# Performance work log

Hardware: AMD Instinct MI355X
Metric: run time of the kernel (lower is better)

## Reference

```python
import jax, jax.numpy as jnp
import numpy as np

GAMMA = 1.5
BN_EPS = 1e-5


def sparsemax(z):
    """Sparsemax along last axis (Martins & Astudillo, 2016)."""
    z = z - jnp.max(z, axis=-1, keepdims=True)
    z_sorted = -jnp.sort(-z, axis=-1)                      # descending sort
    z_cumsum = jnp.cumsum(z_sorted, axis=-1)
    k = jnp.arange(1, z.shape[-1] + 1, dtype=z.dtype)
    support = (z_sorted - (z_cumsum - 1.0) / k) > 0
    k_z = jnp.clip(jnp.sum(support, axis=-1, keepdims=True), 1, None).astype(z.dtype)
    idx = (k_z - 1.0).astype(jnp.int32)
    tau = (jnp.take_along_axis(z_cumsum, idx, axis=-1) - 1.0) / k_z
    return jnp.clip(z - tau, 0.0, None)


def setup_inputs() -> dict:
    key = jax.random.key(0)
    k1, k2 = jax.random.split(key)
    B, T, E, H = 32, 512, 512, 8
    x = jax.random.normal(k1, (B, T, E), dtype=jnp.float32)
    # torch Linear weight (out, in), kaiming-ish scale
    W = jax.random.normal(k2, (H, E, E), dtype=jnp.float32) / np.float32(np.sqrt(E))
    bn_weight = jnp.ones((H, E), dtype=jnp.float32)
    bn_bias = jnp.zeros((H, E), dtype=jnp.float32)
    return {"x": x, "W": W, "bn_weight": bn_weight, "bn_bias": bn_bias}


def reference(x, W, bn_weight, bn_bias):
    B, T, E = x.shape
    H = W.shape[0]
    gi = x.reshape(B * T, E)
    # all-head linear: y[n,o] = sum_i gi[n,i] * W[h,o,i]
    logits = jnp.einsum('ni,hoi->hno', gi, W)              # (H, B*T, E)
    # BatchNorm1d in training mode: batch stats over the B*T axis, biased var
    mean = jnp.mean(logits, axis=1, keepdims=True)
    var = jnp.var(logits, axis=1, keepdims=True)
    logits = (logits - mean) / jnp.sqrt(var + BN_EPS)
    logits = logits * bn_weight[:, None, :] + bn_bias[:, None, :]
    logits = logits.reshape(H, B, T, E)

    prior0 = jnp.ones((B, T, E), dtype=x.dtype)

    def step(prior, logits_h):
        mask_h = sparsemax(logits_h * prior)
        prior = prior * jnp.clip(GAMMA - mask_h, 0.0, None)
        return prior, mask_h

    _, masks = jax.lax.scan(step, prior0, logits)          # masks: (H, B, T, E)
    masked_xs = x[None, :, :, :] * masks                   # (H, B, T, E)
    return masked_xs, jnp.transpose(masks, (1, 0, 2, 3))   # (B, H, T, E)
```

## Files before the change

kernel.cpp:

```cpp
#include <hip/hip_runtime.h>
#include <stdint.h>

#define Hh 8
#define Bb 32
#define Tt 512
#define Ee 512
#define Nn 16384
#define GAMMA_ 1.5f
#define BN_EPS_ 1e-5f

typedef _Float16 f16x4 __attribute__((ext_vector_type(4)));
typedef _Float16 f16x8 __attribute__((ext_vector_type(8)));
typedef float    f32x4 __attribute__((ext_vector_type(4)));

__device__ __forceinline__ void async_ld16(void* lds, const void* g) {
    __builtin_amdgcn_global_load_lds(
        (const __attribute__((address_space(1))) void*)g,
        (__attribute__((address_space(3))) void*)lds, 16, 0, 0);
}

__device__ __forceinline__ float dpp_sum64(float v) {
    int t;
    t = __builtin_amdgcn_update_dpp(0, __float_as_int(v), 0x111, 0xf, 0xf, true);
    v += __int_as_float(t);
    t = __builtin_amdgcn_update_dpp(0, __float_as_int(v), 0x112, 0xf, 0xf, true);
    v += __int_as_float(t);
    t = __builtin_amdgcn_update_dpp(0, __float_as_int(v), 0x114, 0xf, 0xf, true);
    v += __int_as_float(t);
    t = __builtin_amdgcn_update_dpp(0, __float_as_int(v), 0x118, 0xf, 0xf, true);
    v += __int_as_float(t);
    t = __builtin_amdgcn_update_dpp(0, __float_as_int(v), 0x142, 0xf, 0xf, true);
    v += __int_as_float(t);
    t = __builtin_amdgcn_update_dpp(0, __float_as_int(v), 0x143, 0xf, 0xf, true);
    v += __int_as_float(t);
    return __int_as_float(__builtin_amdgcn_readlane(__float_as_int(v), 63));
}

__global__ __launch_bounds__(256) void cvt_kernel(const float* __restrict__ x,
                                                  const float* __restrict__ W,
                                                  _Float16* __restrict__ xh,
                                                  _Float16* __restrict__ wh) {
    const int NX = Bb * Tt * Ee;
    int i = (blockIdx.x * 256 + threadIdx.x) * 4;
    if (i < NX) {
        float4 v = *(const float4*)(x + i);
        f16x4 o = {(_Float16)v.x, (_Float16)v.y, (_Float16)v.z, (_Float16)v.w};
        *(f16x4*)(xh + i) = o;
    } else {
        int j = i - NX;
        float4 v = *(const float4*)(W + j);
        f16x4 o = {(_Float16)v.x, (_Float16)v.y, (_Float16)v.z, (_Float16)v.w};
        *(f16x4*)(wh + j) = o;
    }
}

__global__ __launch_bounds__(256) void gemm_kernel(const _Float16* __restrict__ A,
                                                   const _Float16* __restrict__ Bm,
                                                   _Float16* __restrict__ C,
                                                   float* __restrict__ sums,
                                                   float* __restrict__ sumsq) {
    __shared__ alignas(16) _Float16 As[2][128 * 32];
    __shared__ alignas(16) _Float16 Bs[2][128 * 32];
    const int id = blockIdx.x;
    const int g  = id >> 5;
    const int r  = id & 31;
    const int h  = g >> 4;
    const int q  = r & 7;
    const int s  = r >> 3;
    const int mb = ((g & 15) * 8 + (q & 3) * 2 + (s & 1)) * 128;
    const int nb = ((q >> 2) * 2 + (s >> 1)) * 128;

    const int t    = threadIdx.x;
    const int lane = t & 63;
    const int w    = t >> 6;
    const int wm   = (w >> 1) * 64;
    const int wn   = (w & 1) * 64;
    const int quad = lane >> 4;
    const int l16  = lane & 15;

    const int kc = ((t & 3) - ((t >> 3) & 3)) & 3;
    const _Float16* Ap = A + (size_t)(mb + (t >> 2)) * Ee + kc * 8;
    const _Float16* Bp = Bm + (size_t)h * Ee * Ee + (size_t)(nb + (t >> 2)) * Ee + kc * 8;

    f32x4 acc[4][4] = {};

    async_ld16(&As[0][t * 8],        Ap);
    async_ld16(&As[0][2048 + t * 8], Ap + 64 * Ee);
    async_ld16(&Bs[0][t * 8],        Bp);
    async_ld16(&Bs[0][2048 + t * 8], Bp + 64 * Ee);

    const int so = ((quad + (l16 >> 1)) & 3) * 8;

    int buf = 0;
    for (int k0 = 0; k0 < Ee; k0 += 32) {
        __syncthreads();
        if (k0 + 32 < Ee) {
            int nb2 = buf ^ 1;
            async_ld16(&As[nb2][t * 8],        Ap + k0 + 32);
            async_ld16(&As[nb2][2048 + t * 8], Ap + 64 * Ee + k0 + 32);
            async_ld16(&Bs[nb2][t * 8],        Bp + k0 + 32);
            async_ld16(&Bs[nb2][2048 + t * 8], Bp + 64 * Ee + k0 + 32);
        }
        f16x8 a8[4], b8[4];
#pragma unroll
        for (int mt = 0; mt < 4; ++mt)
            a8[mt] = *(const f16x8*)(&As[buf][(wm + mt * 16 + l16) * 32 + so]);
#pragma unroll
        for (int nt = 0; nt < 4; ++nt)
            b8[nt] = *(const f16x8*)(&Bs[buf][(wn + nt * 16 + l16) * 32 + so]);
#pragma unroll
        for (int mt = 0; mt < 4; ++mt)
#pragma unroll
            for (int nt = 0; nt < 4; ++nt)
                acc[mt][nt] = __builtin_amdgcn_mfma_f32_16x16x32_f16(a8[mt], b8[nt], acc[mt][nt], 0, 0, 0);
        buf ^= 1;
    }

#pragma unroll
    for (int nt = 0; nt < 4; ++nt) {
        float sv = 0.f, ss = 0.f;
#pragma unroll
        for (int mt = 0; mt < 4; ++mt)
#pragma unroll
            for (int rr = 0; rr < 4; ++rr) { float v = acc[mt][nt][rr]; sv += v; ss += v * v; }
        sv += __shfl_xor(sv, 16, 64); sv += __shfl_xor(sv, 32, 64);
        ss += __shfl_xor(ss, 16, 64); ss += __shfl_xor(ss, 32, 64);
        if (quad == 0) {
            int col = nb + wn + nt * 16 + l16;
            atomicAdd(&sums[h * Ee + col], sv);
            atomicAdd(&sumsq[h * Ee + col], ss);
        }
    }

    _Float16* Cp = C + (size_t)h * Nn * Ee;
#pragma unroll
    for (int mt = 0; mt < 4; ++mt)
#pragma unroll
        for (int rr = 0; rr < 4; ++rr) {
            int row = mb + wm + mt * 16 + quad * 4 + rr;
            size_t off = (size_t)row * Ee + nb + wn + l16;
#pragma unroll
            for (int nt = 0; nt < 4; ++nt)
                Cp[off + nt * 16] = (_Float16)acc[mt][nt][rr];
        }
}

__global__ __launch_bounds__(256) void stats_kernel(const float* __restrict__ sums,
                                                    const float* __restrict__ sumsq,
                                                    const float* __restrict__ bnw,
                                                    const float* __restrict__ bnb,
                                                    float* __restrict__ cA,
                                                    float* __restrict__ cB) {
    int i = blockIdx.x * 256 + threadIdx.x;
    float mean = sums[i] * (1.0f / Nn);
    float var  = sumsq[i] * (1.0f / Nn) - mean * mean;
    float inv  = rsqrtf(var + BN_EPS_);
    float a    = bnw[i] * inv;
    cA[i] = a;
    cB[i] = bnb[i] - mean * a;
}

__global__ __launch_bounds__(256) void rows_kernel(const float* __restrict__ x,
                                                   const _Float16* __restrict__ lg,
                                                   const float* __restrict__ cA,
                                                   const float* __restrict__ cB,
                                                   float* __restrict__ out) {
    const int n    = blockIdx.x * 4 + (threadIdx.x >> 6);
    const int lane = threadIdx.x & 63;
    const int e0   = lane * 4;
    const int bb   = n >> 9;
    const int tt   = n & 511;

    float xr[8], prior[8];
    {
        const float* xp = x + (size_t)n * Ee;
        float4 x0 = *(const float4*)(xp + e0);
        float4 x1 = *(const float4*)(xp + 256 + e0);
        xr[0]=x0.x; xr[1]=x0.y; xr[2]=x0.z; xr[3]=x0.w;
        xr[4]=x1.x; xr[5]=x1.y; xr[6]=x1.z; xr[7]=x1.w;
    }
#pragma unroll
    for (int j = 0; j < 8; ++j) prior[j] = 1.0f;

    float* omx = out;
    float* omk = out + (size_t)Hh * Nn * Ee;

    const _Float16* lrow = lg + (size_t)n * Ee;
    f16x4 l0 = *(const f16x4*)(lrow + e0);
    f16x4 l1 = *(const f16x4*)(lrow + 256 + e0);

#pragma unroll 1
    for (int h = 0; h < Hh; ++h) {
        f16x4 p0 = l0, p1 = l1;
        if (h + 1 < Hh) {
            const _Float16* lnx = lrow + (size_t)(h + 1) * Nn * Ee;
            p0 = *(const f16x4*)(lnx + e0);
            p1 = *(const f16x4*)(lnx + 256 + e0);
        }
        float z[8];
        {
            const float* ap = cA + h * Ee + e0;
            const float* bp = cB + h * Ee + e0;
            float4 a0 = *(const float4*)(ap);
            float4 b0 = *(const float4*)(bp);
            float4 a1 = *(const float4*)(ap + 256);
            float4 b1 = *(const float4*)(bp + 256);
            z[0] = ((float)l0[0] * a0.x + b0.x) * prior[0];
            z[1] = ((float)l0[1] * a0.y + b0.y) * prior[1];
            z[2] = ((float)l0[2] * a0.z + b0.z) * prior[2];
            z[3] = ((float)l0[3] * a0.w + b0.w) * prior[3];
            z[4] = ((float)l1[0] * a1.x + b1.x) * prior[4];
            z[5] = ((float)l1[1] * a1.y + b1.y) * prior[5];
            z[6] = ((float)l1[2] * a1.z + b1.z) * prior[6];
            z[7] = ((float)l1[3] * a1.w + b1.w) * prior[7];
        }

        float sl = 0.f;
#pragma unroll
        for (int j = 0; j < 8; ++j) sl += z[j];
        float tau = (dpp_sum64(sl) - 1.0f) * (1.0f / 512.0f);
        int cprev = 512;
#pragma unroll 1
        for (int it = 0; it < 64; ++it) {
            float s2 = 0.f;
            int cnt = 0;
#pragma unroll
            for (int j = 0; j < 8; ++j) {
                bool p = z[j] > tau;
                s2 += p ? z[j] : 0.0f;
                cnt += (int)__popcll(__ballot(p));
            }
            float S = dpp_sum64(s2);
            if (cnt == cprev) break;
            cprev = cnt;
            tau = (S - 1.0f) / (float)cnt;
        }

        size_t oxoff = ((size_t)h * Nn + n) * Ee + e0;
        size_t okoff = (((size_t)bb * Hh + h) * Tt + tt) * Ee + e0;
        f32x4 vx, vm;
#pragma unroll
        for (int j = 0; j < 4; ++j) {
            float m = fmaxf(z[j] - tau, 0.0f);
            prior[j] *= fmaxf(GAMMA_ - m, 0.0f);
            vm[j] = m; vx[j] = xr[j] * m;
        }
        __builtin_nontemporal_store(vx, (f32x4*)(omx + oxoff));
        __builtin_nontemporal_store(vm, (f32x4*)(omk + okoff));
#pragma unroll
        for (int j = 0; j < 4; ++j) {
            float m = fmaxf(z[4 + j] - tau, 0.0f);
            prior[4 + j] *= fmaxf(GAMMA_ - m, 0.0f);
            vm[j] = m; vx[j] = xr[4 + j] * m;
        }
        __builtin_nontemporal_store(vx, (f32x4*)(omx + oxoff + 256));
        __builtin_nontemporal_store(vm, (f32x4*)(omk + okoff + 256));
        l0 = p0; l1 = p1;
    }
}

extern "C" void kernel_launch(void* const* d_in, const int* in_sizes, int n_in,
                              void* d_out, int out_size, void* d_ws, size_t ws_size,
                              hipStream_t stream) {
    const float* x   = (const float*)d_in[0];
    const float* W   = (const float*)d_in[1];
    const float* bnw = (const float*)d_in[2];
    const float* bnb = (const float*)d_in[3];
    float* out = (float*)d_out;

    uint8_t* ws = (uint8_t*)d_ws;
    _Float16* xh = (_Float16*)(ws);
    _Float16* wh = (_Float16*)(ws + 16777216);
    _Float16* lg = (_Float16*)(ws + 20971520);
    float* sums  = (float*)(ws + 155189248);
    float* sumsq = (float*)(ws + 155205632);
    float* cA    = (float*)(ws + 155222016);
    float* cB    = (float*)(ws + 155238400);

    hipMemsetAsync(sums, 0, 2 * 4096 * sizeof(float), stream);

    cvt_kernel<<<10240, 256, 0, stream>>>(x, W, xh, wh);
    gemm_kernel<<<4096, 256, 0, stream>>>(xh, wh, lg, sums, sumsq);
    stats_kernel<<<16, 256, 0, stream>>>(sums, sumsq, bnw, bnb, cA, cB);
    rows_kernel<<<4096, 256, 0, stream>>>(x, lg, cA, cB, out);
}
```

Before: 671.8 us.

## Enlarge GEMM block tile to 256x256 with 512 threads and 128x64 warp tiles

The GEMM moves from a 128x128 block tile with 256 threads to a 256x256 block tile with 512 threads. Each wave now computes a 128x64 sub-tile with 8x4 MFMA accumulators, which raises reuse of each LDS load and cuts global/L2 traffic per FLOP. The cost is more accumulator registers (launch_bounds 512,2), more LDS per block, and fewer blocks (1024), which may lower occupancy. The L2-friendly block swizzle is also replaced with a simple linear mapping.

```diff
diff --git a/kernel.cpp b/kernel.cpp
--- a/kernel.cpp
+++ b/kernel.cpp
@@ -54,27 +54,24 @@
     }
 }
 
-__global__ __launch_bounds__(256) void gemm_kernel(const _Float16* __restrict__ A,
-                                                   const _Float16* __restrict__ Bm,
-                                                   _Float16* __restrict__ C,
-                                                   float* __restrict__ sums,
-                                                   float* __restrict__ sumsq) {
-    __shared__ alignas(16) _Float16 As[2][128 * 32];
-    __shared__ alignas(16) _Float16 Bs[2][128 * 32];
-    const int id = blockIdx.x;
-    const int g  = id >> 5;
-    const int r  = id & 31;
-    const int h  = g >> 4;
-    const int q  = r & 7;
-    const int s  = r >> 3;
-    const int mb = ((g & 15) * 8 + (q & 3) * 2 + (s & 1)) * 128;
-    const int nb = ((q >> 2) * 2 + (s >> 1)) * 128;
+__global__ __launch_bounds__(512, 2) void gemm_kernel(const _Float16* __restrict__ A,
+                                                      const _Float16* __restrict__ Bm,
+                                                      _Float16* __restrict__ C,
+                                                      float* __restrict__ sums,
+                                                      float* __restrict__ sumsq) {
+    __shared__ alignas(16) _Float16 As[2][256 * 32];
+    __shared__ alignas(16) _Float16 Bs[2][256 * 32];
+    const int id  = blockIdx.x;
+    const int h   = id >> 7;
+    const int rem = id & 127;
+    const int mb  = (rem >> 1) * 256;
+    const int nb  = (rem & 1) * 256;
 
     const int t    = threadIdx.x;
     const int lane = t & 63;
     const int w    = t >> 6;
-    const int wm   = (w >> 1) * 64;
-    const int wn   = (w & 1) * 64;
+    const int wrow = (w >> 2) * 128;
+    const int wcol = (w & 3) * 64;
     const int quad = lane >> 4;
     const int l16  = lane & 15;
 
@@ -82,12 +79,12 @@
     const _Float16* Ap = A + (size_t)(mb + (t >> 2)) * Ee + kc * 8;
     const _Float16* Bp = Bm + (size_t)h * Ee * Ee + (size_t)(nb + (t >> 2)) * Ee + kc * 8;
 
-    f32x4 acc[4][4] = {};
+    f32x4 acc[8][4] = {};
 
     async_ld16(&As[0][t * 8],        Ap);
-    async_ld16(&As[0][2048 + t * 8], Ap + 64 * Ee);
+    async_ld16(&As[0][4096 + t * 8], Ap + 128 * Ee);
     async_ld16(&Bs[0][t * 8],        Bp);
-    async_ld16(&Bs[0][2048 + t * 8], Bp + 64 * Ee);
+    async_ld16(&Bs[0][4096 + t * 8], Bp + 128 * Ee);
 
     const int so = ((quad + (l16 >> 1)) & 3) * 8;
 
@@ -95,24 +92,23 @@
     for (int k0 = 0; k0 < Ee; k0 += 32) {
         __syncthreads();
         if (k0 + 32 < Ee) {
-            int nb2 = buf ^ 1;
-            async_ld16(&As[nb2][t * 8],        Ap + k0 + 32);
-            async_ld16(&As[nb2][2048 + t * 8], Ap + 64 * Ee + k0 + 32);
-            async_ld16(&Bs[nb2][t * 8],        Bp + k0 + 32);
-            async_ld16(&Bs[nb2][2048 + t * 8], Bp + 64 * Ee + k0 + 32);
-        }
-        f16x8 a8[4], b8[4];
-#pragma unroll
-        for (int mt = 0; mt < 4; ++mt)
-            a8[mt] = *(const f16x8*)(&As[buf][(wm + mt * 16 + l16) * 32 + so]);
+            int nx = buf ^ 1;
+            async_ld16(&As[nx][t * 8],        Ap + k0 + 32);
+            async_ld16(&As[nx][4096 + t * 8], Ap + 128 * Ee + k0 + 32);
+            async_ld16(&Bs[nx][t * 8],        Bp + k0 + 32);
+            async_ld16(&Bs[nx][4096 + t * 8], Bp + 128 * Ee + k0 + 32);
+        }
+        f16x8 b8[4];
 #pragma unroll
         for (int nt = 0; nt < 4; ++nt)
-            b8[nt] = *(const f16x8*)(&Bs[buf][(wn + nt * 16 + l16) * 32 + so]);
-#pragma unroll
-        for (int mt = 0; mt < 4; ++mt)
+            b8[nt] = *(const f16x8*)(&Bs[buf][(wcol + nt * 16 + l16) * 32 + so]);
+#pragma unroll
+        for (int mt = 0; mt < 8; ++mt) {
+            f16x8 a8 = *(const f16x8*)(&As[buf][(wrow + mt * 16 + l16) * 32 + so]);
 #pragma unroll
             for (int nt = 0; nt < 4; ++nt)
-                acc[mt][nt] = __builtin_amdgcn_mfma_f32_16x16x32_f16(a8[mt], b8[nt], acc[mt][nt], 0, 0, 0);
+                acc[mt][nt] = __builtin_amdgcn_mfma_f32_16x16x32_f16(a8, b8[nt], acc[mt][nt], 0, 0, 0);
+        }
         buf ^= 1;
     }
 
@@ -120,13 +116,13 @@
     for (int nt = 0; nt < 4; ++nt) {
         float sv = 0.f, ss = 0.f;
 #pragma unroll
-        for (int mt = 0; mt < 4; ++mt)
+        for (int mt = 0; mt < 8; ++mt)
 #pragma unroll
             for (int rr = 0; rr < 4; ++rr) { float v = acc[mt][nt][rr]; sv += v; ss += v * v; }
         sv += __shfl_xor(sv, 16, 64); sv += __shfl_xor(sv, 32, 64);
         ss += __shfl_xor(ss, 16, 64); ss += __shfl_xor(ss, 32, 64);
         if (quad == 0) {
-            int col = nb + wn + nt * 16 + l16;
+            int col = nb + wcol + nt * 16 + l16;
             atomicAdd(&sums[h * Ee + col], sv);
             atomicAdd(&sumsq[h * Ee + col], ss);
         }
@@ -134,11 +130,11 @@
 
     _Float16* Cp = C + (size_t)h * Nn * Ee;
 #pragma unroll
-    for (int mt = 0; mt < 4; ++mt)
+    for (int mt = 0; mt < 8; ++mt)
 #pragma unroll
         for (int rr = 0; rr < 4; ++rr) {
-            int row = mb + wm + mt * 16 + quad * 4 + rr;
-            size_t off = (size_t)row * Ee + nb + wn + l16;
+            int row = mb + wrow + mt * 16 + quad * 4 + rr;
+            size_t off = (size_t)row * Ee + nb + wcol + l16;
 #pragma unroll
             for (int nt = 0; nt < 4; ++nt)
                 Cp[off + nt * 16] = (_Float16)acc[mt][nt][rr];
@@ -280,7 +276,7 @@
     hipMemsetAsync(sums, 0, 2 * 4096 * sizeof(float), stream);
 
     cvt_kernel<<<10240, 256, 0, stream>>>(x, W, xh, wh);
-    gemm_kernel<<<4096, 256, 0, stream>>>(xh, wh, lg, sums, sumsq);
+    gemm_kernel<<<1024, 512, 0, stream>>>(xh, wh, lg, sums, sumsq);
     stats_kernel<<<16, 256, 0, stream>>>(sums, sumsq, bnw, bnb, cA, cB);
     rows_kernel<<<4096, 256, 0, stream>>>(x, lg, cA, cB, out);
 }
```

Measured after the change: 656.2 us. 1.02x faster.
